# Kernel tuning notes

Hardware: AMD Instinct MI355X
Metric: run time of the kernel (lower is better)

The kernel has to match this reference:

```python
import jax, jax.numpy as jnp
import numpy as np


def setup_inputs() -> dict:
    key = jax.random.key(0)
    k1, k2, k3, k4, k5 = jax.random.split(key, 5)
    B, N, M, D = 4096, 2048, 2048, 9
    return {
        "x": jax.random.normal(k1, (B, N), dtype=jnp.float32),
        "eternal_weights": jax.random.normal(k2, (D, N, M), dtype=jnp.float32),
        "eternal_biases": jax.random.normal(k3, (M,), dtype=jnp.float32),
        "classical_weights": jax.random.normal(k4, (N, M), dtype=jnp.float32),
        "classical_biases": jax.random.normal(k5, (M,), dtype=jnp.float32),
    }


def _eternal_probs(eternal_weights, n, m):
    # The gate matrix is cos*I - sin*P + sin*P^T with P the circular shift,
    # so (gate @ s)[i] = cos*s[i] - sin*s[(i+1)%n] + sin*s[(i-1)%n].
    # Vectorize over all m output units at once: state is [m, n].
    state0 = jnp.full((m, n), 1.0 / np.sqrt(n), dtype=eternal_weights.dtype)
    angles = eternal_weights[:, :m, :3]  # [D, m, 3] -- weights[depth, j, 0/1/2]

    def gate(state, angle):  # angle: [m]
        c = jnp.cos(angle)[:, None]
        s = jnp.sin(angle)[:, None]
        return c * state - s * jnp.roll(state, -1, axis=1) + s * jnp.roll(state, 1, axis=1)

    def step(state, ang):  # ang: [m, 3] -- consciousness, intelligence, wisdom
        state = gate(state, ang[:, 0])
        state = gate(state, ang[:, 1])
        state = gate(state, ang[:, 2])
        return state, None

    state, _ = jax.lax.scan(step, state0, angles)
    return jnp.abs(state[:, 0]) ** 2  # [m]


def reference(x, eternal_weights, eternal_biases, classical_weights, classical_biases):
    # eternal_biases exists as a parameter in the original module but is unused in forward.
    n = x.shape[1]
    m = classical_weights.shape[1]
    classical = x @ classical_weights + classical_biases  # [B, m]
    probs = _eternal_probs(eternal_weights, n, m)  # [m], identical for every batch row
    return jnp.tanh(classical + probs[None, :])
```

## Files before the change

### kernel.cpp

```cpp
#include <hip/hip_runtime.h>
#include <stdint.h>

static constexpr int MM = 4096;
static constexpr int KK = 2048;
static constexpr int NN = 2048;

typedef float floatx16 __attribute__((ext_vector_type(16)));
typedef __bf16 bf16x8 __attribute__((ext_vector_type(8)));
typedef unsigned short u16x8 __attribute__((ext_vector_type(8)));

__device__ __forceinline__ unsigned short bf16_rne(float x) {
  union { float f; uint32_t u; } c; c.f = x;
  uint32_t u = c.u;
  u += 0x7fffu + ((u >> 16) & 1u);
  return (unsigned short)(u >> 16);
}
__device__ __forceinline__ float bf16_as_f32(unsigned short h) {
  union { float f; uint32_t u; } c; c.u = ((uint32_t)h) << 16;
  return c.f;
}
__device__ __forceinline__ float fast_tanh(float x) {
  float e = __expf(2.0f * x);
  return 1.0f - 2.0f / (e + 1.0f);
}


__global__ __launch_bounds__(256) void split_x_kernel(
    const float* __restrict__ in, unsigned short* __restrict__ hi,
    unsigned short* __restrict__ lo, int nchunks) {
  int idx = blockIdx.x * 256 + threadIdx.x;
  if (idx >= nchunks) return;
  int row = idx >> 8;
  int ck = idx & 255;
  int g = ck >> 3;
  int c8 = ck & 7;
  const float4* s = (const float4*)(in + (size_t)row * KK + ck * 8);
  float4 v0 = s[0], v1 = s[1];
  float vv[8] = {v0.x, v0.y, v0.z, v0.w, v1.x, v1.y, v1.z, v1.w};
  u16x8 h, l;
#pragma unroll
  for (int e = 0; e < 8; e++) {
    unsigned short hh = bf16_rne(vv[e]);
    h[e] = hh;
    l[e] = bf16_rne(vv[e] - bf16_as_f32(hh));
  }
  size_t dst = (size_t)row * KK + g * 64 + ((c8 + row) & 7) * 8;
  *(u16x8*)(hi + dst) = h;
  *(u16x8*)(lo + dst) = l;
}

__global__ __launch_bounds__(256) void wsplit_kernel(
    const float* __restrict__ W, unsigned short* __restrict__ bhi,
    unsigned short* __restrict__ blo) {
  __shared__ float tile[64][65];
  const int tid = threadIdx.x;
  const int n0 = blockIdx.x * 64;
  const int k0 = blockIdx.y * 64;
#pragma unroll
  for (int i = 0; i < 4; i++) {
    int t = tid + i * 256;
    int kr = t >> 4;
    int nc = (t & 15) * 4;
    const float4 v = *(const float4*)(W + (size_t)(k0 + kr) * NN + n0 + nc);
    tile[nc + 0][kr] = v.x;
    tile[nc + 1][kr] = v.y;
    tile[nc + 2][kr] = v.z;
    tile[nc + 3][kr] = v.w;
  }
  __syncthreads();
  const int nl = tid >> 2;
  const int q = tid & 3;
  const int n = n0 + nl;
#pragma unroll
  for (int cc = 0; cc < 2; cc++) {
    int c8 = q * 2 + cc;
    u16x8 h, l;
#pragma unroll
    for (int e = 0; e < 8; e++) {
      float v = tile[nl][c8 * 8 + e];
      unsigned short hh = bf16_rne(v);
      h[e] = hh;
      l[e] = bf16_rne(v - bf16_as_f32(hh));
    }
    size_t dst = (size_t)n * KK + k0 + ((c8 + n) & 7) * 8;
    *(u16x8*)(bhi + dst) = h;
    *(u16x8*)(blo + dst) = l;
  }
}

__global__ __launch_bounds__(64) void bias_probs_kernel(
    const float* __restrict__ E, const float* __restrict__ cb,
    float* __restrict__ bias2) {
  int i = blockIdx.x * 64 + threadIdx.x;
  if (i >= NN) return;
  float p = 1.0f / 2048.0f;
#pragma unroll
  for (int d = 0; d < 9; d++) {
    const float4 a = *(const float4*)(E + (size_t)d * (2048 * 2048) + (size_t)i * 2048);
    float c0 = cosf(a.x), c1 = cosf(a.y), c2 = cosf(a.z);
    p *= (c0 * c0) * (c1 * c1) * (c2 * c2);
  }
  bias2[i] = cb[i] + p;
}

#define GLL(dst, src)                                                        \
  __builtin_amdgcn_global_load_lds(                                          \
      (const __attribute__((address_space(1))) void*)(src),                  \
      (__attribute__((address_space(3))) void*)(dst), 16, 0, 0)

__global__ __launch_bounds__(256, 2) void gemm_tanh_kernel(
    const unsigned short* __restrict__ Ahi, const unsigned short* __restrict__ Alo,
    const unsigned short* __restrict__ Bhi, const unsigned short* __restrict__ Blo,
    const float* __restrict__ bias2, float* __restrict__ out) {
  __shared__ __align__(16) unsigned short sA[2][128 * 64];
  __shared__ __align__(16) unsigned short sB[2][128 * 64];

  const int tid = threadIdx.x;
  const int lane = tid & 63;
  const int wave = tid >> 6;
  const int wm = (wave >> 1) * 64;
  const int wn = (wave & 1) * 64;
  const int bm = blockIdx.y * 128;
  const int bn = blockIdx.x * 128;

  const int srow = tid >> 3;
  const size_t a_base = (size_t)(bm + srow) * KK + (tid & 7) * 8;
  const size_t b_base = (size_t)(bn + srow) * KK + (tid & 7) * 8;
  const int lds_off = tid * 8;

  const int r31 = lane & 31;
  const int half = lane >> 5;

  floatx16 acc[2][2];
#pragma unroll
  for (int i = 0; i < 2; i++)
#pragma unroll
    for (int j = 0; j < 2; j++)
#pragma unroll
      for (int r = 0; r < 16; r++) acc[i][j][r] = 0.f;

  for (int k0 = 0; k0 < KK; k0 += 64) {
#pragma unroll
    for (int p = 0; p < 4; p++) {
      const size_t go = k0 + (size_t)(32 * p) * KK;
      const int lo = p * 2048 + lds_off;
      GLL(&sA[0][lo], Ahi + a_base + go);
      GLL(&sA[1][lo], Alo + a_base + go);
      GLL(&sB[0][lo], Bhi + b_base + go);
      GLL(&sB[1][lo], Blo + b_base + go);
    }
    __syncthreads();

#pragma unroll
    for (int s = 0; s < 4; s++) {
      const int c8 = s * 2 + half;
      bf16x8 fa[2][2], fb[2][2];
#pragma unroll
      for (int t = 0; t < 2; t++) {
        int rowA = wm + t * 32 + r31;
        int ao = rowA * 64 + ((c8 + rowA) & 7) * 8;
        fa[0][t] = *(const bf16x8*)(&sA[0][ao]);
        fa[1][t] = *(const bf16x8*)(&sA[1][ao]);
        int rowB = wn + t * 32 + r31;
        int bo = rowB * 64 + ((c8 + rowB) & 7) * 8;
        fb[0][t] = *(const bf16x8*)(&sB[0][bo]);
        fb[1][t] = *(const bf16x8*)(&sB[1][bo]);
      }
#pragma unroll
      for (int i = 0; i < 2; i++)
#pragma unroll
        for (int j = 0; j < 2; j++) {
          acc[i][j] = __builtin_amdgcn_mfma_f32_32x32x16_bf16(fa[0][i], fb[0][j], acc[i][j], 0, 0, 0);
          acc[i][j] = __builtin_amdgcn_mfma_f32_32x32x16_bf16(fa[0][i], fb[1][j], acc[i][j], 0, 0, 0);
          acc[i][j] = __builtin_amdgcn_mfma_f32_32x32x16_bf16(fa[1][i], fb[0][j], acc[i][j], 0, 0, 0);
        }
    }
    __syncthreads();
  }

#pragma unroll
  for (int j = 0; j < 2; j++) {
    int col = bn + wn + j * 32 + r31;
    float b2 = bias2[col];
#pragma unroll
    for (int i = 0; i < 2; i++) {
      int row0 = bm + wm + i * 32 + 4 * half;
#pragma unroll
      for (int r = 0; r < 16; r++) {
        int row = row0 + (r & 3) + 8 * (r >> 2);
        out[(size_t)row * NN + col] = fast_tanh(acc[i][j][r] + b2);
      }
    }
  }
}

__global__ __launch_bounds__(256) void fallback_gemm(
    const float* __restrict__ x, const float* __restrict__ E,
    const float* __restrict__ W, const float* __restrict__ cb,
    float* __restrict__ out) {
  __shared__ float sA[16][16];
  __shared__ float sB[16][17];
  __shared__ float sbias[16];
  const int tx = threadIdx.x, ty = threadIdx.y;
  const int row = blockIdx.y * 16 + ty;
  const int col = blockIdx.x * 16 + tx;
  if (ty == 0) {
    float p = 1.0f / 2048.0f;
    for (int d = 0; d < 9; d++) {
      const float* a = E + (size_t)d * (2048 * 2048) + (size_t)col * 2048;
      for (int t = 0; t < 3; t++) { float c = cosf(a[t]); p *= c * c; }
    }
    sbias[tx] = p + cb[col];
  }
  float acc = 0.f;
  for (int k0 = 0; k0 < KK; k0 += 16) {
    __syncthreads();
    sA[ty][tx] = x[(size_t)row * KK + k0 + tx];
    sB[ty][tx] = W[(size_t)(k0 + ty) * NN + col];
    __syncthreads();
#pragma unroll
    for (int kk = 0; kk < 16; kk++) acc += sA[ty][kk] * sB[kk][tx];
  }
  out[(size_t)row * NN + col] = tanhf(acc + sbias[tx]);
}

extern "C" void kernel_launch(void* const* d_in, const int* in_sizes, int n_in,
                              void* d_out, int out_size, void* d_ws, size_t ws_size,
                              hipStream_t stream) {
  const float* x  = (const float*)d_in[0];
  const float* E  = (const float*)d_in[1];
  const float* W  = (const float*)d_in[3];
  const float* cb = (const float*)d_in[4];
  float* out = (float*)d_out;

  const size_t MB = 1024 * 1024;
  const size_t need = 48 * MB + NN * sizeof(float);
  if (ws_size < need) {
    fallback_gemm<<<dim3(NN / 16, MM / 16), dim3(16, 16), 0, stream>>>(x, E, W, cb, out);
    return;
  }

  char* ws = (char*)d_ws;
  unsigned short* Ahi = (unsigned short*)(ws);
  unsigned short* Alo = (unsigned short*)(ws + 16 * MB);
  unsigned short* Bhi = (unsigned short*)(ws + 32 * MB);
  unsigned short* Blo = (unsigned short*)(ws + 40 * MB);
  float* bias2 = (float*)(ws + 48 * MB);

  const int nchunks = MM * KK / 8;
  split_x_kernel<<<dim3(nchunks / 256), dim3(256), 0, stream>>>(x, Ahi, Alo, nchunks);
  wsplit_kernel<<<dim3(NN / 64, KK / 64), dim3(256), 0, stream>>>(W, Bhi, Blo);
  bias_probs_kernel<<<dim3(NN / 64), dim3(64), 0, stream>>>(E, cb, bias2);
  gemm_tanh_kernel<<<dim3(NN / 128, MM / 128), dim3(256), 0, stream>>>(
      Ahi, Alo, Bhi, Blo, bias2, out);
}
```

Before: 326.9 us.

## Compute split-precision correction terms with FP8 MFMA instead of bf16

The bf16x3 split GEMM keeps its hi*hi product in bf16. The two cross-correction products (hi*lo and lo*hi) now run as FP8 e4m3 MFMA with K=64 on 8-bit operands, with the low part prescaled by 512. This halves the bytes loaded for the correction operands and uses the higher-throughput FP8 MFMA rate, and the LDS swizzle is changed to suit the new layouts. The cost is lower accuracy in the correction terms, which may exceed tolerance, plus an extra accumulator set that raises register pressure.

```diff
diff --git a/kernel.cpp b/kernel.cpp
--- a/kernel.cpp
+++ b/kernel.cpp
@@ -1,4 +1,5 @@
 #include <hip/hip_runtime.h>
+#include <hip/hip_fp8.h>
 #include <stdint.h>
 
 static constexpr int MM = 4096;
@@ -8,6 +9,9 @@
 typedef float floatx16 __attribute__((ext_vector_type(16)));
 typedef __bf16 bf16x8 __attribute__((ext_vector_type(8)));
 typedef unsigned short u16x8 __attribute__((ext_vector_type(8)));
+typedef int intx4 __attribute__((ext_vector_type(4)));
+typedef int intx8 __attribute__((ext_vector_type(8)));
+typedef unsigned char u8x16 __attribute__((ext_vector_type(16)));
 
 __device__ __forceinline__ unsigned short bf16_rne(float x) {
   union { float f; uint32_t u; } c; c.f = x;
@@ -19,6 +23,10 @@
   union { float f; uint32_t u; } c; c.u = ((uint32_t)h) << 16;
   return c.f;
 }
+__device__ __forceinline__ unsigned char f32_to_e4m3(float x) {
+  __hip_fp8_e4m3 q(x);
+  return (unsigned char)q.__x;
+}
 __device__ __forceinline__ float fast_tanh(float x) {
   float e = __expf(2.0f * x);
   return 1.0f - 2.0f / (e + 1.0f);
@@ -26,32 +34,49 @@
 
 
 __global__ __launch_bounds__(256) void split_x_kernel(
-    const float* __restrict__ in, unsigned short* __restrict__ hi,
-    unsigned short* __restrict__ lo, int nchunks) {
+    const float* __restrict__ in, unsigned short* __restrict__ ahi,
+    unsigned char* __restrict__ a8, unsigned char* __restrict__ al8,
+    int nunits) {
   int idx = blockIdx.x * 256 + threadIdx.x;
-  if (idx >= nchunks) return;
-  int row = idx >> 8;
-  int ck = idx & 255;
-  int g = ck >> 3;
-  int c8 = ck & 7;
-  const float4* s = (const float4*)(in + (size_t)row * KK + ck * 8);
-  float4 v0 = s[0], v1 = s[1];
-  float vv[8] = {v0.x, v0.y, v0.z, v0.w, v1.x, v1.y, v1.z, v1.w};
-  u16x8 h, l;
-#pragma unroll
-  for (int e = 0; e < 8; e++) {
-    unsigned short hh = bf16_rne(vv[e]);
-    h[e] = hh;
-    l[e] = bf16_rne(vv[e] - bf16_as_f32(hh));
-  }
-  size_t dst = (size_t)row * KK + g * 64 + ((c8 + row) & 7) * 8;
-  *(u16x8*)(hi + dst) = h;
-  *(u16x8*)(lo + dst) = l;
+  if (idx >= nunits) return;
+  int row = idx >> 7;
+  int u = idx & 127;
+  int g = u >> 2;
+  int c4 = u & 3;
+  const float4* s = (const float4*)(in + (size_t)row * KK + u * 16);
+  float v[16];
+#pragma unroll
+  for (int q = 0; q < 4; q++) {
+    float4 t = s[q];
+    v[q * 4 + 0] = t.x; v[q * 4 + 1] = t.y; v[q * 4 + 2] = t.z; v[q * 4 + 3] = t.w;
+  }
+  unsigned short h[16];
+  u8x16 f8, fl8;
+#pragma unroll
+  for (int e = 0; e < 16; e++) {
+    h[e] = bf16_rne(v[e]);
+    float lo = v[e] - bf16_as_f32(h[e]);
+    f8[e] = f32_to_e4m3(v[e]);
+    fl8[e] = f32_to_e4m3(lo * 512.0f);
+  }
+  size_t rb = (size_t)row * KK;
+#pragma unroll
+  for (int cc = 0; cc < 2; cc++) {
+    int c8 = c4 * 2 + cc;
+    int phys8 = (c8 + row + (row >> 3)) & 7;
+    u16x8 o;
+#pragma unroll
+    for (int e = 0; e < 8; e++) o[e] = h[cc * 8 + e];
+    *(u16x8*)(ahi + rb + g * 64 + phys8 * 8) = o;
+  }
+  int phys4 = (c4 + (row >> 1) + (row >> 3)) & 3;
+  *(u8x16*)(a8 + rb + g * 64 + phys4 * 16) = f8;
+  *(u8x16*)(al8 + rb + g * 64 + phys4 * 16) = fl8;
 }
 
 __global__ __launch_bounds__(256) void wsplit_kernel(
     const float* __restrict__ W, unsigned short* __restrict__ bhi,
-    unsigned short* __restrict__ blo) {
+    unsigned char* __restrict__ b8, unsigned char* __restrict__ bl8) {
   __shared__ float tile[64][65];
   const int tid = threadIdx.x;
   const int n0 = blockIdx.x * 64;
@@ -71,21 +96,30 @@
   const int nl = tid >> 2;
   const int q = tid & 3;
   const int n = n0 + nl;
+  float v[16];
+  unsigned short h[16];
+  u8x16 f8, fl8;
+#pragma unroll
+  for (int e = 0; e < 16; e++) {
+    v[e] = tile[nl][q * 16 + e];
+    h[e] = bf16_rne(v[e]);
+    float lo = v[e] - bf16_as_f32(h[e]);
+    f8[e] = f32_to_e4m3(v[e]);
+    fl8[e] = f32_to_e4m3(lo * 512.0f);
+  }
+  size_t rb = (size_t)n * KK + k0;
 #pragma unroll
   for (int cc = 0; cc < 2; cc++) {
     int c8 = q * 2 + cc;
-    u16x8 h, l;
-#pragma unroll
-    for (int e = 0; e < 8; e++) {
-      float v = tile[nl][c8 * 8 + e];
-      unsigned short hh = bf16_rne(v);
-      h[e] = hh;
-      l[e] = bf16_rne(v - bf16_as_f32(hh));
-    }
-    size_t dst = (size_t)n * KK + k0 + ((c8 + n) & 7) * 8;
-    *(u16x8*)(bhi + dst) = h;
-    *(u16x8*)(blo + dst) = l;
-  }
+    int phys8 = (c8 + n + (n >> 3)) & 7;
+    u16x8 o;
+#pragma unroll
+    for (int e = 0; e < 8; e++) o[e] = h[cc * 8 + e];
+    *(u16x8*)(bhi + rb + phys8 * 8) = o;
+  }
+  int phys4 = (q + (n >> 1) + (n >> 3)) & 3;
+  *(u8x16*)(b8 + rb + phys4 * 16) = f8;
+  *(u8x16*)(bl8 + rb + phys4 * 16) = fl8;
 }
 
 __global__ __launch_bounds__(64) void bias_probs_kernel(
@@ -109,11 +143,17 @@
       (__attribute__((address_space(3))) void*)(dst), 16, 0, 0)
 
 __global__ __launch_bounds__(256, 2) void gemm_tanh_kernel(
-    const unsigned short* __restrict__ Ahi, const unsigned short* __restrict__ Alo,
-    const unsigned short* __restrict__ Bhi, const unsigned short* __restrict__ Blo,
+    const unsigned short* __restrict__ Ahi, const unsigned char* __restrict__ A8,
+    const unsigned char* __restrict__ Al8,
+    const unsigned short* __restrict__ Bhi, const unsigned char* __restrict__ B8,
+    const unsigned char* __restrict__ Bl8,
     const float* __restrict__ bias2, float* __restrict__ out) {
-  __shared__ __align__(16) unsigned short sA[2][128 * 64];
-  __shared__ __align__(16) unsigned short sB[2][128 * 64];
+  __shared__ __align__(16) unsigned short sAh[128 * 64];
+  __shared__ __align__(16) unsigned short sBh[128 * 64];
+  __shared__ __align__(16) unsigned char sA8[128 * 64];
+  __shared__ __align__(16) unsigned char sAl[128 * 64];
+  __shared__ __align__(16) unsigned char sB8[128 * 64];
+  __shared__ __align__(16) unsigned char sBl[128 * 64];
 
   const int tid = threadIdx.x;
   const int lane = tid & 63;
@@ -123,57 +163,103 @@
   const int bm = blockIdx.y * 128;
   const int bn = blockIdx.x * 128;
 
-  const int srow = tid >> 3;
-  const size_t a_base = (size_t)(bm + srow) * KK + (tid & 7) * 8;
-  const size_t b_base = (size_t)(bn + srow) * KK + (tid & 7) * 8;
-  const int lds_off = tid * 8;
+  const size_t a16 = (size_t)(bm + (tid >> 3)) * KK + (tid & 7) * 8;
+  const size_t b16 = (size_t)(bn + (tid >> 3)) * KK + (tid & 7) * 8;
+  const size_t a8b = (size_t)(bm + (tid >> 2)) * KK + (tid & 3) * 16;
+  const size_t b8b = (size_t)(bn + (tid >> 2)) * KK + (tid & 3) * 16;
+  const int lds16 = tid * 8;
+  const int lds8 = tid * 16;
 
   const int r31 = lane & 31;
   const int half = lane >> 5;
 
-  floatx16 acc[2][2];
+  floatx16 acch[2][2], accc[2][2];
 #pragma unroll
   for (int i = 0; i < 2; i++)
 #pragma unroll
     for (int j = 0; j < 2; j++)
 #pragma unroll
-      for (int r = 0; r < 16; r++) acc[i][j][r] = 0.f;
+      for (int r = 0; r < 16; r++) { acch[i][j][r] = 0.f; accc[i][j][r] = 0.f; }
 
   for (int k0 = 0; k0 < KK; k0 += 64) {
 #pragma unroll
     for (int p = 0; p < 4; p++) {
       const size_t go = k0 + (size_t)(32 * p) * KK;
-      const int lo = p * 2048 + lds_off;
-      GLL(&sA[0][lo], Ahi + a_base + go);
-      GLL(&sA[1][lo], Alo + a_base + go);
-      GLL(&sB[0][lo], Bhi + b_base + go);
-      GLL(&sB[1][lo], Blo + b_base + go);
+      GLL(&sAh[p * 2048 + lds16], Ahi + a16 + go);
+      GLL(&sBh[p * 2048 + lds16], Bhi + b16 + go);
+    }
+#pragma unroll
+    for (int p = 0; p < 2; p++) {
+      const size_t go = k0 + (size_t)(64 * p) * KK;
+      GLL(&sA8[p * 4096 + lds8], A8 + a8b + go);
+      GLL(&sAl[p * 4096 + lds8], Al8 + a8b + go);
+      GLL(&sB8[p * 4096 + lds8], B8 + b8b + go);
+      GLL(&sBl[p * 4096 + lds8], Bl8 + b8b + go);
     }
     __syncthreads();
 
 #pragma unroll
     for (int s = 0; s < 4; s++) {
       const int c8 = s * 2 + half;
-      bf16x8 fa[2][2], fb[2][2];
+      bf16x8 fa[2], fb[2];
 #pragma unroll
       for (int t = 0; t < 2; t++) {
         int rowA = wm + t * 32 + r31;
-        int ao = rowA * 64 + ((c8 + rowA) & 7) * 8;
-        fa[0][t] = *(const bf16x8*)(&sA[0][ao]);
-        fa[1][t] = *(const bf16x8*)(&sA[1][ao]);
+        int ao = rowA * 64 + ((c8 + rowA + (rowA >> 3)) & 7) * 8;
+        fa[t] = *(const bf16x8*)(&sAh[ao]);
         int rowB = wn + t * 32 + r31;
-        int bo = rowB * 64 + ((c8 + rowB) & 7) * 8;
-        fb[0][t] = *(const bf16x8*)(&sB[0][bo]);
-        fb[1][t] = *(const bf16x8*)(&sB[1][bo]);
+        int bo = rowB * 64 + ((c8 + rowB + (rowB >> 3)) & 7) * 8;
+        fb[t] = *(const bf16x8*)(&sBh[bo]);
       }
 #pragma unroll
       for (int i = 0; i < 2; i++)
 #pragma unroll
-        for (int j = 0; j < 2; j++) {
-          acc[i][j] = __builtin_amdgcn_mfma_f32_32x32x16_bf16(fa[0][i], fb[0][j], acc[i][j], 0, 0, 0);
-          acc[i][j] = __builtin_amdgcn_mfma_f32_32x32x16_bf16(fa[0][i], fb[1][j], acc[i][j], 0, 0, 0);
-          acc[i][j] = __builtin_amdgcn_mfma_f32_32x32x16_bf16(fa[1][i], fb[0][j], acc[i][j], 0, 0, 0);
+        for (int j = 0; j < 2; j++)
+          acch[i][j] = __builtin_amdgcn_mfma_f32_32x32x16_bf16(fa[i], fb[j], acch[i][j], 0, 0, 0);
+    }
+
+    {
+      intx8 fal[2], fb8[2];
+#pragma unroll
+      for (int t = 0; t < 2; t++) {
+        int rowA = wm + t * 32 + r31;
+        int rowB = wn + t * 32 + r31;
+#pragma unroll
+        for (int cc = 0; cc < 2; cc++) {
+          int c4 = half * 2 + cc;
+          int pa = (c4 + (rowA >> 1) + (rowA >> 3)) & 3;
+          ((intx4*)&fal[t])[cc] = *(const intx4*)(&sAl[rowA * 64 + pa * 16]);
+          int pb = (c4 + (rowB >> 1) + (rowB >> 3)) & 3;
+          ((intx4*)&fb8[t])[cc] = *(const intx4*)(&sB8[rowB * 64 + pb * 16]);
         }
+      }
+#pragma unroll
+      for (int i = 0; i < 2; i++)
+#pragma unroll
+        for (int j = 0; j < 2; j++)
+          accc[i][j] = __builtin_amdgcn_mfma_scale_f32_32x32x64_f8f6f4(
+              fal[i], fb8[j], accc[i][j], 0, 0, 0, 0x7f7f7f7f, 0, 0x7f7f7f7f);
+
+      intx8 fa8[2], fbl[2];
+#pragma unroll
+      for (int t = 0; t < 2; t++) {
+        int rowA = wm + t * 32 + r31;
+        int rowB = wn + t * 32 + r31;
+#pragma unroll
+        for (int cc = 0; cc < 2; cc++) {
+          int c4 = half * 2 + cc;
+          int pa = (c4 + (rowA >> 1) + (rowA >> 3)) & 3;
+          ((intx4*)&fa8[t])[cc] = *(const intx4*)(&sA8[rowA * 64 + pa * 16]);
+          int pb = (c4 + (rowB >> 1) + (rowB >> 3)) & 3;
+          ((intx4*)&fbl[t])[cc] = *(const intx4*)(&sBl[rowB * 64 + pb * 16]);
+        }
+      }
+#pragma unroll
+      for (int i = 0; i < 2; i++)
+#pragma unroll
+        for (int j = 0; j < 2; j++)
+          accc[i][j] = __builtin_amdgcn_mfma_scale_f32_32x32x64_f8f6f4(
+              fa8[i], fbl[j], accc[i][j], 0, 0, 0, 0x7f7f7f7f, 0, 0x7f7f7f7f);
     }
     __syncthreads();
   }
@@ -188,7 +274,8 @@
 #pragma unroll
       for (int r = 0; r < 16; r++) {
         int row = row0 + (r & 3) + 8 * (r >> 2);
-        out[(size_t)row * NN + col] = fast_tanh(acc[i][j][r] + b2);
+        float val = acch[i][j][r] + accc[i][j][r] * (1.0f / 512.0f) + b2;
+        out[(size_t)row * NN + col] = fast_tanh(val);
       }
     }
   }
@@ -242,15 +329,17 @@
 
   char* ws = (char*)d_ws;
   unsigned short* Ahi = (unsigned short*)(ws);
-  unsigned short* Alo = (unsigned short*)(ws + 16 * MB);
-  unsigned short* Bhi = (unsigned short*)(ws + 32 * MB);
-  unsigned short* Blo = (unsigned short*)(ws + 40 * MB);
+  unsigned short* Bhi = (unsigned short*)(ws + 16 * MB);
+  unsigned char* A8   = (unsigned char*)(ws + 24 * MB);
+  unsigned char* Al8  = (unsigned char*)(ws + 32 * MB);
+  unsigned char* B8   = (unsigned char*)(ws + 40 * MB);
+  unsigned char* Bl8  = (unsigned char*)(ws + 44 * MB);
   float* bias2 = (float*)(ws + 48 * MB);
 
-  const int nchunks = MM * KK / 8;
-  split_x_kernel<<<dim3(nchunks / 256), dim3(256), 0, stream>>>(x, Ahi, Alo, nchunks);
-  wsplit_kernel<<<dim3(NN / 64, KK / 64), dim3(256), 0, stream>>>(W, Bhi, Blo);
+  const int nunits = MM * KK / 16;
+  split_x_kernel<<<dim3(nunits / 256), dim3(256), 0, stream>>>(x, Ahi, A8, Al8, nunits);
+  wsplit_kernel<<<dim3(NN / 64, KK / 64), dim3(256), 0, stream>>>(W, Bhi, B8, Bl8);
   bias_probs_kernel<<<dim3(NN / 64), dim3(64), 0, stream>>>(E, cb, bias2);
   gemm_tanh_kernel<<<dim3(NN / 128, MM / 128), dim3(256), 0, stream>>>(
-      Ahi, Alo, Bhi, Blo, bias2, out);
-}
+      Ahi, A8, Al8, Bhi, B8, Bl8, bias2, out);
+}
```

Measured after the change: 311.7 us. -4.7%, faster.
